# Performance work log

Hardware: AMD Instinct MI355X
Metric: run time of the kernel (lower is better)

The kernel has to match this reference:

```python
import jax, jax.numpy as jnp
import numpy as np

DIM = 192
HEADS = 6
EMB4 = 192  # embed_dim * 4

def layer_norm(x, g, b, eps=1e-5):
    mu = jnp.mean(x, axis=-1, keepdims=True)
    var = jnp.var(x, axis=-1, keepdims=True)
    return (x - mu) * jax.lax.rsqrt(var + eps) * g + b

def setup_inputs() -> dict:
    key = jax.random.key(0)
    ks = jax.random.split(key, 8)
    B, C, H, W = 4, DIM, 128, 128
    M = 256
    s = lambda fan: 1.0 / np.sqrt(fan)
    return {
        "x": jax.random.normal(ks[0], (B, C, H, W), jnp.float32),
        "prior": jax.random.normal(ks[1], (B, M, EMB4), jnp.float32),
        "ln1_g": jnp.ones((DIM,), jnp.float32),
        "ln1_b": jnp.zeros((DIM,), jnp.float32),
        "ln2_g": jnp.ones((EMB4,), jnp.float32),
        "ln2_b": jnp.zeros((EMB4,), jnp.float32),
        "Wq": jax.random.normal(ks[2], (DIM, DIM), jnp.float32) * s(DIM),
        "Wkv": jax.random.normal(ks[3], (EMB4, 2 * DIM), jnp.float32) * s(EMB4),
        "Wp": jax.random.normal(ks[4], (DIM, DIM), jnp.float32) * s(DIM),
        "bp": jnp.zeros((DIM,), jnp.float32),
    }

def reference(x, prior, ln1_g, ln1_b, ln2_g, ln2_b, Wq, Wkv, Wp, bp):
    B, C, H, W = x.shape
    nh = HEADS
    hd = C // nh
    scale = hd ** (-0.5)
    xt = x.reshape(B, C, H * W).transpose(0, 2, 1)  # b n c
    _x = layer_norm(xt, ln1_g, ln1_b)
    pr = layer_norm(prior, ln2_g, ln2_b)
    q = _x @ Wq                      # b n (h d)
    kv = pr @ Wkv                    # b m (2 h d)
    k, v = jnp.split(kv, 2, axis=-1)
    N = H * W
    Mlen = prior.shape[1]
    q = q.reshape(B, N, nh, hd).transpose(0, 2, 1, 3)      # b h n d
    k = k.reshape(B, Mlen, nh, hd).transpose(0, 2, 1, 3)   # b h m d
    v = v.reshape(B, Mlen, nh, hd).transpose(0, 2, 1, 3)   # b h m d
    attn = jnp.einsum('bhnd,bhmd->bhnm', q, k) * scale
    attn = jax.nn.softmax(attn, axis=-1)
    out = jnp.einsum('bhnm,bhmd->bhnd', attn, v)
    out = out.transpose(0, 2, 1, 3).reshape(B, N, C)
    out = out @ Wp + bp
    y = xt + out
    return y.transpose(0, 2, 1).reshape(B, C, H, W)
```

## Files before the change

kernel.cpp:

```cpp
#include <hip/hip_runtime.h>

typedef unsigned short u16;
typedef unsigned int u32;

#define C_DIM 192
#define N_TOK 16384
#define M_LEN 256
#define HD 32
#define NH 6

#define AF_STRIDE 3080

typedef __attribute__((ext_vector_type(8))) short short8v;
typedef __attribute__((ext_vector_type(4))) float float4v;

__device__ __forceinline__ u32 cvt_pk_bf16(float lo, float hi) {
    u32 r;
    asm("v_cvt_pk_bf16_f32 %0, %1, %2" : "=v"(r) : "v"(lo), "v"(hi));
    return r;
}
__device__ __forceinline__ u16 f2bf_hw(float f) {
    return (u16)cvt_pk_bf16(f, f);
}

__global__ __launch_bounds__(256) void w_prep2(
    const float* __restrict__ Wq, u16* __restrict__ WqF,
    const float* __restrict__ Wp, u16* __restrict__ WpF)
{
    int bb = blockIdx.x;
    const float* W = (bb < 18) ? Wq : Wp;
    u16* outp = (bb < 18) ? WqF : WpF;
    int gt = (bb % 18) * 256 + threadIdx.x;
    int f = gt >> 6, lane = gt & 63;
    int q8 = lane >> 4, ln = lane & 15;
    int wv = f / 18, r = f % 18;
    int kt = r / 3, jj = r % 3;
    const float* w0 = W + (kt * 32 + q8 * 8) * C_DIM + (wv * 3 + jj) * 16 + ln;
    union { u32 w[4]; short8v v; } out;
#pragma unroll
    for (int j = 0; j < 4; ++j)
        out.w[j] = cvt_pk_bf16(w0[(2 * j) * C_DIM], w0[(2 * j + 1) * C_DIM]);
    *(short8v*)&outp[f * 512 + lane * 8] = out.v;
}

__global__ __launch_bounds__(256) void ln1_q_mfma(
    const float* __restrict__ x, const float* __restrict__ g,
    const float* __restrict__ beta, const u16* __restrict__ WqF,
    u16* __restrict__ q)
{
    __shared__ u16 Af[4 * AF_STRIDE];
    __shared__ u16 Tq[64 * 200];
    __shared__ float part[64][4][2];
    __shared__ float mu_s[64], rs_s[64];
    int b = blockIdx.x >> 8;
    int n0 = (blockIdx.x & 255) * 64;
    int t = threadIdx.x;
    int wv = t >> 6, lane = t & 63;

    float xv[48];
    {
        const float* xb = x + (((size_t)(b * C_DIM + wv * 48)) << 14) + n0 + lane;
        float s1 = 0.f, s2 = 0.f;
#pragma unroll
        for (int i = 0; i < 48; ++i) {
            float f = xb[(size_t)i << 14];
            xv[i] = f; s1 += f; s2 += f * f;
        }
        part[lane][wv][0] = s1; part[lane][wv][1] = s2;
    }
    __syncthreads();
    if (t < 64) {
        float a  = part[t][0][0] + part[t][1][0] + part[t][2][0] + part[t][3][0];
        float c2 = part[t][0][1] + part[t][1][1] + part[t][2][1] + part[t][3][1];
        float mu = a * (1.f / C_DIM);
        mu_s[t] = mu;
        rs_s[t] = rsqrtf(c2 * (1.f / C_DIM) - mu * mu + 1e-5f);
    }
    __syncthreads();

    {
        float mu = mu_s[lane], rs = rs_s[lane];
        int mt2 = lane >> 4, ln2 = lane & 15;
        u32* A32 = (u32*)Af;
#pragma unroll
        for (int i = 0; i < 48; i += 2) {
            int c = wv * 48 + i;
            float f0 = (xv[i]     - mu) * rs * g[c]     + beta[c];
            float f1 = (xv[i + 1] - mu) * rs * g[c + 1] + beta[c + 1];
            int kt = c >> 5, k8 = (c & 31) >> 3, j = c & 7;
            A32[(mt2 * AF_STRIDE + kt * 512 + k8 * 128 + ln2 * 8 + j) >> 1] =
                cvt_pk_bf16(f0, f1);
        }
    }
    __syncthreads();

    int q8 = lane >> 4, ln = lane & 15;
    short8v Bf[18];
#pragma unroll
    for (int i = 0; i < 18; ++i)
        Bf[i] = *(const short8v*)&WqF[(wv * 18 + i) * 512 + lane * 8];

#pragma unroll
    for (int mt = 0; mt < 4; ++mt) {
        float4v acc[3] = {{0.f,0.f,0.f,0.f},{0.f,0.f,0.f,0.f},{0.f,0.f,0.f,0.f}};
#pragma unroll
        for (int kt = 0; kt < 6; ++kt) {
            short8v a = *(const short8v*)&Af[mt * AF_STRIDE + kt * 512 + lane * 8];
#pragma unroll
            for (int jj = 0; jj < 3; ++jj)
                acc[jj] = __builtin_amdgcn_mfma_f32_16x16x32_bf16(a, Bf[kt * 3 + jj], acc[jj], 0, 0, 0);
        }
#pragma unroll
        for (int jj = 0; jj < 3; ++jj)
#pragma unroll
            for (int r = 0; r < 4; ++r)
                Tq[(mt * 16 + q8 * 4 + r) * 200 + (wv * 3 + jj) * 16 + ln] = f2bf_hw(acc[jj][r]);
    }
    __syncthreads();

    {
        int tok = t >> 2, pp = t & 3;
        const uint4* src = (const uint4*)&Tq[tok * 200 + pp * 48];
        uint4* dst = (uint4*)(q + ((size_t)(b * N_TOK + n0 + tok)) * C_DIM + pp * 48);
#pragma unroll
        for (int i = 0; i < 6; ++i) dst[i] = src[i];
    }
}

__global__ __launch_bounds__(192) void ln2_kv_frag(
    const float* __restrict__ prior, const float* __restrict__ g,
    const float* __restrict__ beta, const float* __restrict__ Wkv,
    u16* __restrict__ KfG, u16* __restrict__ VfG)
{
    __shared__ float pr[C_DIM];
    __shared__ float red[3][2];
    int row = blockIdx.x;
    int tid = threadIdx.x;
    int wv = tid >> 6;
    float val = prior[row * C_DIM + tid];
    float s1 = val, s2 = val * val;
#pragma unroll
    for (int m = 1; m < 64; m <<= 1) {
        s1 += __shfl_xor(s1, m);
        s2 += __shfl_xor(s2, m);
    }
    if ((tid & 63) == 0) { red[wv][0] = s1; red[wv][1] = s2; }
    __syncthreads();
    float a  = red[0][0] + red[1][0] + red[2][0];
    float c2 = red[0][1] + red[1][1] + red[2][1];
    float mu = a * (1.f / C_DIM);
    float rs = rsqrtf(c2 * (1.f / C_DIM) - mu * mu + 1e-5f);
    pr[tid] = (val - mu) * rs * g[tid] + beta[tid];
    __syncthreads();
    float ka = 0.f, va = 0.f;
    for (int c = 0; c < C_DIM; ++c) {
        float p = pr[c];
        ka += p * Wkv[c * 384 + tid];
        va += p * Wkv[c * 384 + 192 + tid];
    }
    int b = row >> 8, m = row & 255;
    int h = tid >> 5, dim = tid & 31;
    int bh = b * NH + h;
    int kt = m >> 4, r = m & 15;
    {
        int qd = dim >> 3, j = dim & 7;
        KfG[bh * 8192 + kt * 512 + (qd * 16 + r) * 8 + j] =
            f2bf_hw(ka * 0.17677669529663687f);
    }
    {
        int qd = r >> 2, reg = r & 3;
        int P = kt >> 1;
        int j = reg + 4 * (kt & 1);
        int dh = dim >> 4, n = dim & 15;
        VfG[bh * 8192 + (P * 2 + dh) * 512 + (qd * 16 + n) * 8 + j] = f2bf_hw(va);
    }
}

__global__ __launch_bounds__(384, 2) void attn_proj_fused(
    const u16* __restrict__ q, const u16* __restrict__ KfG,
    const u16* __restrict__ VfG, const u16* __restrict__ WpF,
    const float* __restrict__ bp, const float* __restrict__ x,
    float* __restrict__ y)
{
    __shared__ float Tf[C_DIM * 68];
    u16* att_lds = (u16*)Tf;
    int b  = blockIdx.x >> 8;
    int n0 = (blockIdx.x & 255) * 64;
    int t = threadIdx.x;
    int wave = t >> 6, lane = t & 63;
    int quad = lane >> 4, ln = lane & 15;
    const float LOG2E = 1.4426950408889634f;

    int h = wave;
    short8v k_r[16], v_r[16];
    {
        const u16* Kf = KfG + (b * NH + h) * 8192;
        const u16* Vf = VfG + (b * NH + h) * 8192;
#pragma unroll
        for (int kt = 0; kt < 16; ++kt)
            k_r[kt] = *(const short8v*)&Kf[kt * 512 + lane * 8];
#pragma unroll
        for (int kt = 0; kt < 16; ++kt)
            v_r[kt] = *(const short8v*)&Vf[kt * 512 + lane * 8];
    }

    {
        const u16* qbase = q + ((size_t)(b * N_TOK + n0 + ln)) * C_DIM + h * HD + quad * 8;
        short8v qnext = *(const short8v*)qbase;

        for (int rep = 0; rep < 4; ++rep) {
            short8v qf = qnext;
            int nrep = rep < 3 ? rep + 1 : 3;
            qnext = *(const short8v*)(qbase + (size_t)nrep * 16 * C_DIM);

            float4v s[16];
#pragma unroll
            for (int kt = 0; kt < 16; ++kt) {
                float4v z = {0.f, 0.f, 0.f, 0.f};
                s[kt] = __builtin_amdgcn_mfma_f32_16x16x32_bf16(k_r[kt], qf, z, 0, 0, 0);
            }

            float mx = fmaxf(fmaxf(s[0][0], s[0][1]), fmaxf(s[0][2], s[0][3]));
#pragma unroll
            for (int kt = 1; kt < 16; ++kt)
                mx = fmaxf(fmaxf(mx, s[kt][0]),
                           fmaxf(s[kt][1], fmaxf(s[kt][2], s[kt][3])));
            mx = fmaxf(mx, __shfl_xor(mx, 16));
            mx = fmaxf(mx, __shfl_xor(mx, 32));

            float nm = -mx * LOG2E;
            float l = 0.f;
#pragma unroll
            for (int kt = 0; kt < 16; ++kt) {
#pragma unroll
                for (int r = 0; r < 4; ++r) {
                    float p = __builtin_amdgcn_exp2f(fmaf(s[kt][r], LOG2E, nm));
                    s[kt][r] = p;
                    l += p;
                }
            }
            l += __shfl_xor(l, 16);
            l += __shfl_xor(l, 32);
            float inv = __builtin_amdgcn_rcpf(l);

            float4v o0 = {0.f, 0.f, 0.f, 0.f}, o1 = {0.f, 0.f, 0.f, 0.f};
#pragma unroll
            for (int P = 0; P < 8; ++P) {
                union { u32 w[4]; short8v v; } pf;
                pf.w[0] = cvt_pk_bf16(s[2 * P][0],     s[2 * P][1]);
                pf.w[1] = cvt_pk_bf16(s[2 * P][2],     s[2 * P][3]);
                pf.w[2] = cvt_pk_bf16(s[2 * P + 1][0], s[2 * P + 1][1]);
                pf.w[3] = cvt_pk_bf16(s[2 * P + 1][2], s[2 * P + 1][3]);
                o0 = __builtin_amdgcn_mfma_f32_16x16x32_bf16(pf.v, v_r[2 * P],     o0, 0, 0, 0);
                o1 = __builtin_amdgcn_mfma_f32_16x16x32_bf16(pf.v, v_r[2 * P + 1], o1, 0, 0, 0);
            }

#pragma unroll
            for (int r = 0; r < 4; ++r) {
                float invr = __shfl(inv, quad * 4 + r);
                u16* rw = &att_lds[(rep * 16 + quad * 4 + r) * 200 + h * HD];
                rw[ln]      = f2bf_hw(o0[r] * invr);
                rw[16 + ln] = f2bf_hw(o1[r] * invr);
            }
        }
    }
    __syncthreads();

    float4 xu[8];
    {
        int r0 = t >> 4, p = t & 15;
#pragma unroll
        for (int pass = 0; pass < 8; ++pass) {
            int c = pass * 24 + r0;
            xu[pass] = ((const float4*)(x + (((size_t)(b * C_DIM + c)) << 14) + n0))[p];
        }
    }

    short8v Bf[12];
#pragma unroll
    for (int jc = 0; jc < 2; ++jc) {
        int cf = wave * 2 + jc;
        int wv = cf / 3, jj = cf % 3;
#pragma unroll
        for (int kt = 0; kt < 6; ++kt)
            Bf[jc * 6 + kt] = *(const short8v*)&WpF[(wv * 18 + kt * 3 + jj) * 512 + lane * 8];
    }

    float4v acc[4][2];
#pragma unroll
    for (int mt = 0; mt < 4; ++mt) {
#pragma unroll
        for (int jc = 0; jc < 2; ++jc) {
            float4v z = {0.f, 0.f, 0.f, 0.f};
            acc[mt][jc] = z;
        }
#pragma unroll
        for (int kt = 0; kt < 6; ++kt) {
            short8v a = *(const short8v*)&att_lds[(mt * 16 + ln) * 200 + quad * 8 + kt * 32];
#pragma unroll
            for (int jc = 0; jc < 2; ++jc)
                acc[mt][jc] = __builtin_amdgcn_mfma_f32_16x16x32_bf16(a, Bf[jc * 6 + kt], acc[mt][jc], 0, 0, 0);
        }
    }
    __syncthreads();

#pragma unroll
    for (int mt = 0; mt < 4; ++mt)
#pragma unroll
        for (int jc = 0; jc < 2; ++jc) {
            int c = (wave * 2 + jc) * 16 + ln;
#pragma unroll
            for (int r = 0; r < 4; ++r)
                Tf[c * 68 + mt * 16 + quad * 4 + r] = acc[mt][jc][r];
        }
    __syncthreads();

    {
        int r0 = t >> 4;
        int p  = t & 15;
#pragma unroll
        for (int pass = 0; pass < 8; ++pass) {
            int c = pass * 24 + r0;
            float bias = bp[c];
            float4 a = *(const float4*)&Tf[c * 68 + p * 4];
            float4*       yr = (float4*)(y + (((size_t)(b * C_DIM + c)) << 14) + n0);
            float4 u = xu[pass];
            float4 w;
            w.x = a.x + bias + u.x;
            w.y = a.y + bias + u.y;
            w.z = a.z + bias + u.z;
            w.w = a.w + bias + u.w;
            yr[p] = w;
        }
    }
}

__global__ __launch_bounds__(256) void attn_mfma_kernel(
    const u16* __restrict__ q, const u16* __restrict__ KfG,
    const u16* __restrict__ VfG, u16* __restrict__ att)
{
    __shared__ u16 sh[16384];
    int tb = blockIdx.x & 63;
    int bh = blockIdx.x >> 6;
    int h = bh % NH, b = bh / NH;
    int tid = threadIdx.x;
    int wave = tid >> 6, lane = tid & 63;
    int quad = lane >> 4, ln = lane & 15;

    const u16* qbase = q + ((size_t)(b * N_TOK + tb * 256 + wave * 16 + ln)) * C_DIM
                         + h * HD + quad * 8;
    short8v qnext = *(const short8v*)qbase;

    {
        const uint4* Ks = (const uint4*)(KfG + bh * 8192);
        const uint4* Vs = (const uint4*)(VfG + bh * 8192);
        uint4* d = (uint4*)sh;
#pragma unroll
        for (int i = tid; i < 2048; i += 256)
            d[i] = (i < 1024) ? Ks[i] : Vs[i - 1024];
    }
    __syncthreads();

    const u16* Kf = sh;
    const u16* Vf = sh + 8192;
    const float LOG2E = 1.4426950408889634f;

    for (int rep = 0; rep < 4; ++rep) {
        short8v qf = qnext;
        int nrep = rep < 3 ? rep + 1 : 3;
        qnext = *(const short8v*)(qbase + (size_t)nrep * 64 * C_DIM);

        float4v s[16];
#pragma unroll
        for (int kt = 0; kt < 16; ++kt) {
            short8v kf = *(const short8v*)&Kf[kt * 512 + lane * 8];
            float4v z = {0.f, 0.f, 0.f, 0.f};
            s[kt] = __builtin_amdgcn_mfma_f32_16x16x32_bf16(kf, qf, z, 0, 0, 0);
        }

        float mx = fmaxf(fmaxf(s[0][0], s[0][1]), fmaxf(s[0][2], s[0][3]));
#pragma unroll
        for (int kt = 1; kt < 16; ++kt)
            mx = fmaxf(fmaxf(mx, s[kt][0]),
                       fmaxf(s[kt][1], fmaxf(s[kt][2], s[kt][3])));
        mx = fmaxf(mx, __shfl_xor(mx, 16));
        mx = fmaxf(mx, __shfl_xor(mx, 32));

        float nm = -mx * LOG2E;
        float l = 0.f;
#pragma unroll
        for (int kt = 0; kt < 16; ++kt) {
#pragma unroll
            for (int r = 0; r < 4; ++r) {
                float p = __builtin_amdgcn_exp2f(fmaf(s[kt][r], LOG2E, nm));
                s[kt][r] = p;
                l += p;
            }
        }
        l += __shfl_xor(l, 16);
        l += __shfl_xor(l, 32);
        float inv = __builtin_amdgcn_rcpf(l);

        float4v o0 = {0.f, 0.f, 0.f, 0.f}, o1 = {0.f, 0.f, 0.f, 0.f};
#pragma unroll
        for (int P = 0; P < 8; ++P) {
            union { u32 w[4]; short8v v; } pf;
            pf.w[0] = cvt_pk_bf16(s[2 * P][0],     s[2 * P][1]);
            pf.w[1] = cvt_pk_bf16(s[2 * P][2],     s[2 * P][3]);
            pf.w[2] = cvt_pk_bf16(s[2 * P + 1][0], s[2 * P + 1][1]);
            pf.w[3] = cvt_pk_bf16(s[2 * P + 1][2], s[2 * P + 1][3]);
            short8v v0 = *(const short8v*)&Vf[(P * 2 + 0) * 512 + lane * 8];
            short8v v1 = *(const short8v*)&Vf[(P * 2 + 1) * 512 + lane * 8];
            o0 = __builtin_amdgcn_mfma_f32_16x16x32_bf16(pf.v, v0, o0, 0, 0, 0);
            o1 = __builtin_amdgcn_mfma_f32_16x16x32_bf16(pf.v, v1, o1, 0, 0, 0);
        }

        int token0 = tb * 256 + rep * 64 + wave * 16;
#pragma unroll
        for (int r = 0; r < 4; ++r) {
            float invr = __shfl(inv, quad * 4 + r);
            u16* row = att + ((size_t)(b * N_TOK + token0 + quad * 4 + r)) * C_DIM + h * HD;
            row[ln]      = f2bf_hw(o0[r] * invr);
            row[16 + ln] = f2bf_hw(o1[r] * invr);
        }
    }
}

__global__ __launch_bounds__(256) void proj_res_mfma(
    const u16* __restrict__ att, const float* __restrict__ Wp,
    const u16* __restrict__ WpF, const float* __restrict__ bp,
    const float* __restrict__ x, float* __restrict__ y)
{
    __shared__ float Tf[C_DIM * 68];
    int b = blockIdx.x >> 8;
    int n0 = (blockIdx.x & 255) * 64;
    int t = threadIdx.x;
    int wv = t >> 6, lane = t & 63;
    int q8 = lane >> 4, ln = lane & 15;

    short8v Bf[18];
    if (WpF) {
#pragma unroll
        for (int i = 0; i < 18; ++i)
            Bf[i] = *(const short8v*)&WpF[(wv * 18 + i) * 512 + lane * 8];
    } else {
#pragma unroll
        for (int kt = 0; kt < 6; ++kt) {
#pragma unroll
            for (int jj = 0; jj < 3; ++jj) {
                const float* w0 = Wp + (kt * 32 + q8 * 8) * C_DIM + (wv * 3 + jj) * 16 + ln;
                union { u32 w[4]; short8v v; } f;
#pragma unroll
                for (int wj = 0; wj < 4; ++wj)
                    f.w[wj] = cvt_pk_bf16(w0[(2 * wj) * C_DIM], w0[(2 * wj + 1) * C_DIM]);
                Bf[kt * 3 + jj] = f.v;
            }
        }
    }

#pragma unroll
    for (int mt = 0; mt < 4; ++mt) {
        const u16* ab = att + ((size_t)(b * N_TOK + n0 + mt * 16 + ln)) * C_DIM + q8 * 8;
        float4v acc[3] = {{0.f,0.f,0.f,0.f},{0.f,0.f,0.f,0.f},{0.f,0.f,0.f,0.f}};
#pragma unroll
        for (int kt = 0; kt < 6; ++kt) {
            short8v a = *(const short8v*)(ab + kt * 32);
#pragma unroll
            for (int jj = 0; jj < 3; ++jj)
                acc[jj] = __builtin_amdgcn_mfma_f32_16x16x32_bf16(a, Bf[kt * 3 + jj], acc[jj], 0, 0, 0);
        }
#pragma unroll
        for (int jj = 0; jj < 3; ++jj)
#pragma unroll
            for (int r = 0; r < 4; ++r)
                Tf[((wv * 3 + jj) * 16 + ln) * 68 + mt * 16 + q8 * 4 + r] = acc[jj][r];
    }
    __syncthreads();

    {
        int r0 = t >> 4;
        int p  = t & 15;
#pragma unroll
        for (int pass = 0; pass < 12; ++pass) {
            int c = pass * 16 + r0;
            float bias = bp[c];
            float4 a = *(const float4*)&Tf[c * 68 + p * 4];
            const float4* xr = (const float4*)(x + (((size_t)(b * C_DIM + c)) << 14) + n0);
            float4*       yr = (float4*)(y + (((size_t)(b * C_DIM + c)) << 14) + n0);
            float4 u = xr[p];
            float4 w;
            w.x = a.x + bias + u.x;
            w.y = a.y + bias + u.y;
            w.z = a.z + bias + u.z;
            w.w = a.w + bias + u.w;
            yr[p] = w;
        }
    }
}

extern "C" void kernel_launch(void* const* d_in, const int* in_sizes, int n_in,
                              void* d_out, int out_size, void* d_ws, size_t ws_size,
                              hipStream_t stream) {
    const float* x     = (const float*)d_in[0];
    const float* prior = (const float*)d_in[1];
    const float* ln1_g = (const float*)d_in[2];
    const float* ln1_b = (const float*)d_in[3];
    const float* ln2_g = (const float*)d_in[4];
    const float* ln2_b = (const float*)d_in[5];
    const float* Wq    = (const float*)d_in[6];
    const float* Wkv   = (const float*)d_in[7];
    const float* Wp    = (const float*)d_in[8];
    const float* bp    = (const float*)d_in[9];

    char* outc = (char*)d_out;
    float* y = (float*)d_out;

    const size_t needF = 25165824ull + 393216ull + 393216ull + 73728ull;
    if (ws_size >= needF) {
        char* wsc = (char*)d_ws;
        u16* qb  = (u16*)wsc;
        u16* KfG = (u16*)(wsc + 25165824);
        u16* VfG = (u16*)(wsc + 25165824 + 393216);
        u16* WpF = (u16*)(wsc + 25165824 + 786432);
        u16* WqF = (u16*)outc;

        w_prep2<<<36, 256, 0, stream>>>(Wq, WqF, Wp, WpF);
        ln1_q_mfma<<<1024, 256, 0, stream>>>(x, ln1_g, ln1_b, WqF, qb);
        ln2_kv_frag<<<1024, 192, 0, stream>>>(prior, ln2_g, ln2_b, Wkv, KfG, VfG);
        attn_proj_fused<<<1024, 384, 0, stream>>>(qb, KfG, VfG, WpF, bp, x, y);
    } else {
        u16*   qb   = (u16*)outc;
        u16*   WqF  = (u16*)(outc + 26738688);
        u16*   KfG  = (u16*)(outc + 26812416);
        u16*   VfG  = (u16*)(outc + 27205632);
        u16*   att  = (u16*)d_ws;
        bool has_wpf = ws_size >= 25165824ull + 73728ull;
        u16* WpF = has_wpf ? (u16*)((char*)d_ws + 25165824) : (u16*)nullptr;

        w_prep2<<<has_wpf ? 36 : 18, 256, 0, stream>>>(Wq, WqF, Wp, has_wpf ? WpF : WqF);
        ln1_q_mfma<<<1024, 256, 0, stream>>>(x, ln1_g, ln1_b, WqF, qb);
        ln2_kv_frag<<<1024, 192, 0, stream>>>(prior, ln2_g, ln2_b, Wkv, KfG, VfG);
        attn_mfma_kernel<<<1536, 256, 0, stream>>>(qb, KfG, VfG, att);
        proj_res_mfma<<<1024, 256, 0, stream>>>(att, Wp, WpF, bp, x, y);
    }
}
```

Baseline: 189.4 us.

## Merge weight prep and LN2/KV projection into one launch; split reduction chains

Weight fragment prep and the prior LayerNorm plus KV projection now run as one combined kernel launch. It uses 256 blocks of 4 rows each instead of the separate 1024-block ln2_kv_frag launch, which removes one kernel launch from the main path. Separately, the LN1 statistics, the softmax max/sum reductions and the PV MFMA accumulators are split into multiple independent partial chains to shorten dependency latency. The cost is more registers in the attention kernel, and the combined prep kernel has fewer blocks, each doing a serial 192-step loop over the reduction dimension.

After: 194.3 us. 2.6% more time.

```diff
diff --git a/kernel.cpp b/kernel.cpp
--- a/kernel.cpp
+++ b/kernel.cpp
@@ -10,6 +10,7 @@
 #define NH 6
 
 #define AF_STRIDE 3080
+#define LN2_BLOCKS 256
 
 typedef __attribute__((ext_vector_type(8))) short short8v;
 typedef __attribute__((ext_vector_type(4))) float float4v;
@@ -23,14 +24,10 @@
     return (u16)cvt_pk_bf16(f, f);
 }
 
-__global__ __launch_bounds__(256) void w_prep2(
-    const float* __restrict__ Wq, u16* __restrict__ WqF,
-    const float* __restrict__ Wp, u16* __restrict__ WpF)
-{
-    int bb = blockIdx.x;
-    const float* W = (bb < 18) ? Wq : Wp;
-    u16* outp = (bb < 18) ? WqF : WpF;
-    int gt = (bb % 18) * 256 + threadIdx.x;
+__device__ __forceinline__ void wprep_block(
+    const float* __restrict__ W, u16* __restrict__ outp, int bb, int tid)
+{
+    int gt = bb * 256 + tid;
     int f = gt >> 6, lane = gt & 63;
     int q8 = lane >> 4, ln = lane & 15;
     int wv = f / 18, r = f % 18;
@@ -41,6 +38,99 @@
     for (int j = 0; j < 4; ++j)
         out.w[j] = cvt_pk_bf16(w0[(2 * j) * C_DIM], w0[(2 * j + 1) * C_DIM]);
     *(short8v*)&outp[f * 512 + lane * 8] = out.v;
+}
+
+__global__ __launch_bounds__(256) void w_prep2(
+    const float* __restrict__ Wq, u16* __restrict__ WqF,
+    const float* __restrict__ Wp, u16* __restrict__ WpF)
+{
+    int bb = blockIdx.x;
+    wprep_block((bb < 18) ? Wq : Wp, (bb < 18) ? WqF : WpF, bb % 18, threadIdx.x);
+}
+
+__global__ __launch_bounds__(256) void prep_combo(
+    const float* __restrict__ prior, const float* __restrict__ g,
+    const float* __restrict__ beta, const float* __restrict__ Wkv,
+    u16* __restrict__ KfG, u16* __restrict__ VfG,
+    const float* __restrict__ Wq, u16* __restrict__ WqF,
+    const float* __restrict__ Wp, u16* __restrict__ WpF)
+{
+    int tid = threadIdx.x;
+    if (blockIdx.x >= LN2_BLOCKS) {
+        int bb = blockIdx.x - LN2_BLOCKS;
+        wprep_block((bb < 18) ? Wq : Wp, (bb < 18) ? WqF : WpF, bb % 18, tid);
+        return;
+    }
+    __shared__ float pr[4][C_DIM];
+    __shared__ float red[4][3][2];
+    int row0 = blockIdx.x * 4;
+    float val[4];
+    if (tid < 192) {
+        int wv = tid >> 6;
+#pragma unroll
+        for (int i = 0; i < 4; ++i) {
+            val[i] = prior[(row0 + i) * C_DIM + tid];
+            float s1 = val[i], s2 = val[i] * val[i];
+#pragma unroll
+            for (int m = 1; m < 64; m <<= 1) {
+                s1 += __shfl_xor(s1, m);
+                s2 += __shfl_xor(s2, m);
+            }
+            if ((tid & 63) == 0) { red[i][wv][0] = s1; red[i][wv][1] = s2; }
+        }
+    }
+    __syncthreads();
+    if (tid < 192) {
+#pragma unroll
+        for (int i = 0; i < 4; ++i) {
+            float a  = red[i][0][0] + red[i][1][0] + red[i][2][0];
+            float c2 = red[i][0][1] + red[i][1][1] + red[i][2][1];
+            float mu = a * (1.f / C_DIM);
+            float rs = rsqrtf(c2 * (1.f / C_DIM) - mu * mu + 1e-5f);
+            pr[i][tid] = (val[i] - mu) * rs * g[tid] + beta[tid];
+        }
+    }
+    __syncthreads();
+    if (tid >= 192) return;
+
+    float ka0[4] = {0,0,0,0}, ka1[4] = {0,0,0,0};
+    float va0[4] = {0,0,0,0}, va1[4] = {0,0,0,0};
+    for (int c = 0; c < C_DIM; c += 2) {
+        float w0k = Wkv[c * 384 + tid];
+        float w1k = Wkv[(c + 1) * 384 + tid];
+        float w0v = Wkv[c * 384 + 192 + tid];
+        float w1v = Wkv[(c + 1) * 384 + 192 + tid];
+#pragma unroll
+        for (int i = 0; i < 4; ++i) {
+            float p0 = pr[i][c], p1 = pr[i][c + 1];
+            ka0[i] = fmaf(p0, w0k, ka0[i]);
+            ka1[i] = fmaf(p1, w1k, ka1[i]);
+            va0[i] = fmaf(p0, w0v, va0[i]);
+            va1[i] = fmaf(p1, w1v, va1[i]);
+        }
+    }
+    int h = tid >> 5, dim = tid & 31;
+#pragma unroll
+    for (int i = 0; i < 4; ++i) {
+        int row = row0 + i;
+        int b = row >> 8, m = row & 255;
+        int bh = b * NH + h;
+        int kt = m >> 4, r = m & 15;
+        float ka = ka0[i] + ka1[i];
+        float va = va0[i] + va1[i];
+        {
+            int qd = dim >> 3, j = dim & 7;
+            KfG[bh * 8192 + kt * 512 + (qd * 16 + r) * 8 + j] =
+                f2bf_hw(ka * 0.17677669529663687f);
+        }
+        {
+            int qd = r >> 2, reg = r & 3;
+            int P = kt >> 1;
+            int j = reg + 4 * (kt & 1);
+            int dh = dim >> 4, n = dim & 15;
+            VfG[bh * 8192 + (P * 2 + dh) * 512 + (qd * 16 + n) * 8 + j] = f2bf_hw(va);
+        }
+    }
 }
 
 __global__ __launch_bounds__(256) void ln1_q_mfma(
@@ -60,13 +150,16 @@
     float xv[48];
     {
         const float* xb = x + (((size_t)(b * C_DIM + wv * 48)) << 14) + n0 + lane;
-        float s1 = 0.f, s2 = 0.f;
+        float s1p[4] = {0,0,0,0}, s2p[4] = {0,0,0,0};
 #pragma unroll
         for (int i = 0; i < 48; ++i) {
             float f = xb[(size_t)i << 14];
-            xv[i] = f; s1 += f; s2 += f * f;
-        }
-        part[lane][wv][0] = s1; part[lane][wv][1] = s2;
+            xv[i] = f;
+            s1p[i & 3] += f;
+            s2p[i & 3] += f * f;
+        }
+        part[lane][wv][0] = (s1p[0] + s1p[1]) + (s1p[2] + s1p[3]);
+        part[lane][wv][1] = (s2p[0] + s2p[1]) + (s2p[2] + s2p[3]);
     }
     __syncthreads();
     if (t < 64) {
@@ -220,30 +313,38 @@
                 s[kt] = __builtin_amdgcn_mfma_f32_16x16x32_bf16(k_r[kt], qf, z, 0, 0, 0);
             }
 
-            float mx = fmaxf(fmaxf(s[0][0], s[0][1]), fmaxf(s[0][2], s[0][3]));
-#pragma unroll
-            for (int kt = 1; kt < 16; ++kt)
-                mx = fmaxf(fmaxf(mx, s[kt][0]),
-                           fmaxf(s[kt][1], fmaxf(s[kt][2], s[kt][3])));
-            mx = fmaxf(mx, __shfl_xor(mx, 16));
+            float mk[16];
+#pragma unroll
+            for (int kt = 0; kt < 16; ++kt)
+                mk[kt] = fmaxf(fmaxf(s[kt][0], s[kt][1]), fmaxf(s[kt][2], s[kt][3]));
+#pragma unroll
+            for (int st = 8; st >= 1; st >>= 1)
+#pragma unroll
+                for (int i = 0; i < st; ++i) mk[i] = fmaxf(mk[i], mk[i + st]);
+            float mx = fmaxf(mk[0], __shfl_xor(mk[0], 16));
             mx = fmaxf(mx, __shfl_xor(mx, 32));
 
             float nm = -mx * LOG2E;
-            float l = 0.f;
+            float lk[16];
 #pragma unroll
             for (int kt = 0; kt < 16; ++kt) {
-#pragma unroll
-                for (int r = 0; r < 4; ++r) {
-                    float p = __builtin_amdgcn_exp2f(fmaf(s[kt][r], LOG2E, nm));
-                    s[kt][r] = p;
-                    l += p;
-                }
+                float p0 = __builtin_amdgcn_exp2f(fmaf(s[kt][0], LOG2E, nm));
+                float p1 = __builtin_amdgcn_exp2f(fmaf(s[kt][1], LOG2E, nm));
+                float p2 = __builtin_amdgcn_exp2f(fmaf(s[kt][2], LOG2E, nm));
+                float p3 = __builtin_amdgcn_exp2f(fmaf(s[kt][3], LOG2E, nm));
+                s[kt][0] = p0; s[kt][1] = p1; s[kt][2] = p2; s[kt][3] = p3;
+                lk[kt] = (p0 + p1) + (p2 + p3);
             }
-            l += __shfl_xor(l, 16);
+#pragma unroll
+            for (int st = 8; st >= 1; st >>= 1)
+#pragma unroll
+                for (int i = 0; i < st; ++i) lk[i] += lk[i + st];
+            float l = lk[0] + __shfl_xor(lk[0], 16);
             l += __shfl_xor(l, 32);
             float inv = __builtin_amdgcn_rcpf(l);
 
-            float4v o0 = {0.f, 0.f, 0.f, 0.f}, o1 = {0.f, 0.f, 0.f, 0.f};
+            float4v o0a = {0.f,0.f,0.f,0.f}, o0b = {0.f,0.f,0.f,0.f};
+            float4v o1a = {0.f,0.f,0.f,0.f}, o1b = {0.f,0.f,0.f,0.f};
 #pragma unroll
             for (int P = 0; P < 8; ++P) {
                 union { u32 w[4]; short8v v; } pf;
@@ -251,9 +352,16 @@
                 pf.w[1] = cvt_pk_bf16(s[2 * P][2],     s[2 * P][3]);
                 pf.w[2] = cvt_pk_bf16(s[2 * P + 1][0], s[2 * P + 1][1]);
                 pf.w[3] = cvt_pk_bf16(s[2 * P + 1][2], s[2 * P + 1][3]);
-                o0 = __builtin_amdgcn_mfma_f32_16x16x32_bf16(pf.v, v_r[2 * P],     o0, 0, 0, 0);
-                o1 = __builtin_amdgcn_mfma_f32_16x16x32_bf16(pf.v, v_r[2 * P + 1], o1, 0, 0, 0);
+                if (P & 1) {
+                    o0b = __builtin_amdgcn_mfma_f32_16x16x32_bf16(pf.v, v_r[2 * P],     o0b, 0, 0, 0);
+                    o1b = __builtin_amdgcn_mfma_f32_16x16x32_bf16(pf.v, v_r[2 * P + 1], o1b, 0, 0, 0);
+                } else {
+                    o0a = __builtin_amdgcn_mfma_f32_16x16x32_bf16(pf.v, v_r[2 * P],     o0a, 0, 0, 0);
+                    o1a = __builtin_amdgcn_mfma_f32_16x16x32_bf16(pf.v, v_r[2 * P + 1], o1a, 0, 0, 0);
+                }
             }
+            float4v o0 = o0a + o0b;
+            float4v o1 = o1a + o1b;
 
 #pragma unroll
             for (int r = 0; r < 4; ++r) {
@@ -524,9 +632,9 @@
         u16* WpF = (u16*)(wsc + 25165824 + 786432);
         u16* WqF = (u16*)outc;
 
-        w_prep2<<<36, 256, 0, stream>>>(Wq, WqF, Wp, WpF);
+        prep_combo<<<LN2_BLOCKS + 36, 256, 0, stream>>>(
+            prior, ln2_g, ln2_b, Wkv, KfG, VfG, Wq, WqF, Wp, WpF);
         ln1_q_mfma<<<1024, 256, 0, stream>>>(x, ln1_g, ln1_b, WqF, qb);
-        ln2_kv_frag<<<1024, 192, 0, stream>>>(prior, ln2_g, ln2_b, Wkv, KfG, VfG);
         attn_proj_fused<<<1024, 384, 0, stream>>>(qb, KfG, VfG, WpF, bp, x, y);
     } else {
         u16*   qb   = (u16*)outc;
```
